# Performance work log

Hardware: AMD Instinct MI355X
Metric: run time of the kernel (lower is better)

Reference implementation:

```python
import jax, jax.numpy as jnp
import numpy as np

C = 32          # mid_channel / in_channel
B = 8           # batch size (number of scenes)
N = 2_000_000   # total points across batch
BN_EPS = 1e-4   # BatchNorm1d eps from norm_fn


def setup_inputs() -> dict:
    key = jax.random.key(0)
    ks = jax.random.split(key, 8)
    s = 0.05
    return {
        "feats": jax.random.normal(ks[0], (N, C), dtype=jnp.float32),
        "batch_idxs": jnp.sort(jax.random.randint(ks[1], (N,), 0, B, dtype=jnp.int32)),
        "off_w1": jax.random.normal(ks[2], (C, C), dtype=jnp.float32) * s,
        "off_b1": jnp.zeros((C,), jnp.float32),
        "bn_gamma": jnp.ones((C,), jnp.float32),   # set_bn_init fills 1.0
        "bn_beta": jnp.zeros((C,), jnp.float32),   # set_bn_init fills 0.0
        "off_w2": jax.random.normal(ks[3], (C, 3), dtype=jnp.float32) * s,
        "off_b2": jnp.zeros((3,), jnp.float32),
        "mask_w1": jax.random.normal(ks[4], (C, C), dtype=jnp.float32) * s,
        "mask_b1": jnp.zeros((C,), jnp.float32),
        "mask_w2": jax.random.normal(ks[5], (C, 1), dtype=jnp.float32) * s,
        "mask_b2": jnp.zeros((1,), jnp.float32),
        "iou_w": jax.random.normal(ks[6], (C, 1), dtype=jnp.float32) * s,
        "iou_b": jnp.zeros((1,), jnp.float32),
    }


def reference(feats, batch_idxs, off_w1, off_b1, bn_gamma, bn_beta, off_w2, off_b2,
              mask_w1, mask_b1, mask_w2, mask_b2, iou_w, iou_b):
    # offset_linear = MLP([C, C, 3], norm_fn=BatchNorm1d): Linear -> BN -> ReLU -> Linear
    h = feats @ off_w1 + off_b1                      # [N, C]
    mu = h.mean(axis=0)
    var = jnp.mean(jnp.square(h - mu), axis=0)       # biased var (torch BN training fwd)
    h = (h - mu) * jax.lax.rsqrt(var + BN_EPS) * bn_gamma + bn_beta
    h = jax.nn.relu(h)
    pt_offsets = h @ off_w2 + off_b2                 # [N, 3]

    # mask_linear = MLP([C, C, 1], norm_fn=None): Linear -> ReLU -> Linear
    m = jax.nn.relu(feats @ mask_w1 + mask_b1)       # [N, C]
    mask_scores = m @ mask_w2 + mask_b2              # [N, 1]

    # global_pool: scatter mean of features over per-batch segments (batch offsets)
    ones = jnp.ones((feats.shape[0],), feats.dtype)
    counts = jax.ops.segment_sum(ones, batch_idxs, num_segments=B)          # [B]
    pooled = jax.ops.segment_sum(feats, batch_idxs, num_segments=B)         # [B, C]
    pooled = pooled / jnp.maximum(counts, 1.0)[:, None]

    # iou_score_linear on the pooled proposal feature
    iou_scores = pooled @ iou_w + iou_b              # [B, 1]
    return pt_offsets, mask_scores, pooled, iou_scores
```

## Files before the change

### kernel.cpp

```cpp
#include <hip/hip_runtime.h>

#define TPB 256

typedef __attribute__((ext_vector_type(8))) short short8;
typedef __attribute__((ext_vector_type(4))) float floatx4;

__device__ __forceinline__ unsigned short bf_rne(float f){
    union { float f; unsigned u; } c; c.f = f;
    unsigned r = c.u + 0x7fffu + ((c.u >> 16) & 1u);
    return (unsigned short)(r >> 16);
}
__device__ __forceinline__ unsigned pack_bf(float lo, float hi){
    union { float f; unsigned u; } a, b; a.f = lo; b.f = hi;
    return __builtin_amdgcn_perm(b.u, a.u, 0x07060302u);
}

__global__ void lb_kernel(const int* __restrict__ bidx, int* __restrict__ ws_lb,
                          int N, int B)
{
    const int t = threadIdx.x;
    if (t <= B){
        int lo = 0, hi = N;
        while (lo < hi){
            const int mid = (lo + hi) >> 1;
            if (bidx[mid] < t) lo = mid + 1; else hi = mid;
        }
        ws_lb[t] = lo;
    }
}

__global__ __launch_bounds__(TPB) void pass1_kernel(
    const float* __restrict__ feats, const int* __restrict__ ws_lb,
    const float* __restrict__ w1, const float* __restrict__ b1,
    const float* __restrict__ mw1, const float* __restrict__ mb1,
    const float* __restrict__ mw2, const float* __restrict__ mb2,
    float* __restrict__ mask_out,
    float* __restrict__ ws_sum, float* __restrict__ ws_sq,
    float* __restrict__ ws_pool, int N, int B)
{
    __shared__ float s_stage[TPB/64][1024];
    __shared__ float s_pool[8][32];
    __shared__ float s_sum[32];
    __shared__ float s_sq[32];
    __shared__ int   s_lb[9];

    const int tid  = threadIdx.x;
    const int lane = tid & 63;
    const int wv   = tid >> 6;
    const int p = lane & 15;
    const int q = lane >> 4;

    if (tid < 32){ s_sum[tid] = 0.f; s_sq[tid] = 0.f; }
    ((float*)s_pool)[tid] = 0.f;
    if (tid <= B) s_lb[tid] = ws_lb[tid];
    __syncthreads();

    short8 aw0, aw1, am0, am1;
    floatx4 ci_h0, ci_h1, ci_m0, ci_m1;
    float mw2v[8];
#pragma unroll
    for (int j = 0; j < 8; ++j){
        const int k = q * 8 + j;
        aw0[j] = (short)bf_rne(w1 [k * 32 + p]);
        aw1[j] = (short)bf_rne(w1 [k * 32 + 16 + p]);
        am0[j] = (short)bf_rne(mw1[k * 32 + p]);
        am1[j] = (short)bf_rne(mw1[k * 32 + 16 + p]);
    }
#pragma unroll
    for (int r = 0; r < 4; ++r){
        const int c0 = q * 4 + r, c1 = 16 + q * 4 + r;
        ci_h0[r] = b1[c0];  ci_h1[r] = b1[c1];
        ci_m0[r] = mb1[c0]; ci_m1[r] = mb1[c1];
        mw2v[r] = mw2[c0];  mw2v[4 + r] = mw2[c1];
    }
    const float mb2s = mb2[0];

    float hsum[8] = {0,0,0,0,0,0,0,0};
    float hsq [8] = {0,0,0,0,0,0,0,0};
    float pacc[4] = {0,0,0,0};

    const int ngroups = (N + 31) >> 5;
    const int nw  = gridDim.x * (TPB / 64);
    const int wid = blockIdx.x * (TPB / 64) + wv;
    const int g0  = (int)((long)wid       * ngroups / nw);
    const int gE  = (int)((long)(wid + 1) * ngroups / nw);

    int curb = 0;
    { const int r = g0 << 5; while (curb < B - 1 && r >= s_lb[curb + 1]) curb++; }
    int lbn = s_lb[curb + 1];

    float* sw = &s_stage[wv][0];
    const int wrow  = lane >> 3;
    const int wg    = (lane & 7) ^ wrow;
    const int cbase = (lane & 7) << 2;
    const int wo0 = ( 0 + wrow) * 32 + (wg << 2);
    const int wo1 = ( 8 + wrow) * 32 + (wg << 2);
    const int wo2 = (16 + wrow) * 32 + (wg << 2);
    const int wo3 = (24 + wrow) * 32 + (wg << 2);
    const int e = p & 7;
    const int ra0 = p * 32        + ((((q << 1)    ) ^ e) << 2);
    const int ra1 = p * 32        + ((((q << 1) + 1) ^ e) << 2);
    const int rb0 = (16 + p) * 32 + ((((q << 1)    ) ^ e) << 2);
    const int rb1 = (16 + p) * 32 + ((((q << 1) + 1) ^ e) << 2);

    floatx4 sv0 = {0,0,0,0}, sv1 = {0,0,0,0}, sv2 = {0,0,0,0}, sv3 = {0,0,0,0};
    if (g0 < gE){
        const float* gp = feats + ((size_t)g0 << 10) + (lane << 2);
        const int r = (g0 << 5) + wrow;
        if (r + 24 < N){
            sv0 = *(const floatx4*)(gp);
            sv1 = *(const floatx4*)(gp + 256);
            sv2 = *(const floatx4*)(gp + 512);
            sv3 = *(const floatx4*)(gp + 768);
        } else {
            if (r      < N) sv0 = *(const floatx4*)(gp);
            if (r +  8 < N) sv1 = *(const floatx4*)(gp + 256);
            if (r + 16 < N) sv2 = *(const floatx4*)(gp + 512);
            if (r + 24 < N) sv3 = *(const floatx4*)(gp + 768);
        }
    }

    for (int g = g0; g < gE; ++g){
        *(floatx4*)(sw + wo0) = sv0;
        *(floatx4*)(sw + wo1) = sv1;
        *(floatx4*)(sw + wo2) = sv2;
        *(floatx4*)(sw + wo3) = sv3;

        floatx4 nv0 = {0,0,0,0}, nv1 = {0,0,0,0}, nv2 = {0,0,0,0}, nv3 = {0,0,0,0};
        if (g + 1 < gE){
            const float* gp = feats + ((size_t)(g + 1) << 10) + (lane << 2);
            const int r = ((g + 1) << 5) + wrow;
            if (r + 24 < N){
                nv0 = *(const floatx4*)(gp);
                nv1 = *(const floatx4*)(gp + 256);
                nv2 = *(const floatx4*)(gp + 512);
                nv3 = *(const floatx4*)(gp + 768);
            } else {
                if (r      < N) nv0 = *(const floatx4*)(gp);
                if (r +  8 < N) nv1 = *(const floatx4*)(gp + 256);
                if (r + 16 < N) nv2 = *(const floatx4*)(gp + 512);
                if (r + 24 < N) nv3 = *(const floatx4*)(gp + 768);
            }
        }

        const int r0 = g << 5;
        if (r0 >= lbn){
#pragma unroll
            for (int j = 0; j < 4; ++j){
                if (pacc[j] != 0.f) atomicAdd(&s_pool[curb][cbase + j], pacc[j]);
                pacc[j] = 0.f;
            }
            do { curb++; } while (curb < B - 1 && r0 >= s_lb[curb + 1]);
            lbn = s_lb[curb + 1];
        }
        const bool slow = (r0 + 31 >= lbn) || (r0 + 31 >= N);

        if (!slow){
            pacc[0] += sv0[0] + sv1[0] + sv2[0] + sv3[0];
            pacc[1] += sv0[1] + sv1[1] + sv2[1] + sv3[1];
            pacc[2] += sv0[2] + sv1[2] + sv2[2] + sv3[2];
            pacc[3] += sv0[3] + sv1[3] + sv2[3] + sv3[3];
        } else {
#define SLOWROW(SV, L) { \
            const int row = r0 + (L * 8) + wrow; \
            if (row < N){ \
                int bl = curb; \
                for (int c = curb + 1; c < B; ++c) bl += (row >= s_lb[c]); \
                atomicAdd(&s_pool[bl][cbase + 0], SV[0]); \
                atomicAdd(&s_pool[bl][cbase + 1], SV[1]); \
                atomicAdd(&s_pool[bl][cbase + 2], SV[2]); \
                atomicAdd(&s_pool[bl][cbase + 3], SV[3]); \
            } }
            SLOWROW(sv0, 0) SLOWROW(sv1, 1) SLOWROW(sv2, 2) SLOWROW(sv3, 3)
#undef SLOWROW
        }

        const floatx4 vA0 = *(const floatx4*)(sw + ra0);
        const floatx4 vA1 = *(const floatx4*)(sw + ra1);
        const floatx4 vB0 = *(const floatx4*)(sw + rb0);
        const floatx4 vB1 = *(const floatx4*)(sw + rb1);

        short8 bfA, bfB;
        {
            unsigned* ba = (unsigned*)&bfA;
            ba[0] = pack_bf(vA0[0], vA0[1]); ba[1] = pack_bf(vA0[2], vA0[3]);
            ba[2] = pack_bf(vA1[0], vA1[1]); ba[3] = pack_bf(vA1[2], vA1[3]);
            unsigned* bb = (unsigned*)&bfB;
            bb[0] = pack_bf(vB0[0], vB0[1]); bb[1] = pack_bf(vB0[2], vB0[3]);
            bb[2] = pack_bf(vB1[0], vB1[1]); bb[3] = pack_bf(vB1[2], vB1[3]);
        }

        const floatx4 chA0 = __builtin_amdgcn_mfma_f32_16x16x32_bf16(aw0, bfA, ci_h0, 0, 0, 0);
        const floatx4 chA1 = __builtin_amdgcn_mfma_f32_16x16x32_bf16(aw1, bfA, ci_h1, 0, 0, 0);
        const floatx4 cmA0 = __builtin_amdgcn_mfma_f32_16x16x32_bf16(am0, bfA, ci_m0, 0, 0, 0);
        const floatx4 cmA1 = __builtin_amdgcn_mfma_f32_16x16x32_bf16(am1, bfA, ci_m1, 0, 0, 0);
        const floatx4 chB0 = __builtin_amdgcn_mfma_f32_16x16x32_bf16(aw0, bfB, ci_h0, 0, 0, 0);
        const floatx4 chB1 = __builtin_amdgcn_mfma_f32_16x16x32_bf16(aw1, bfB, ci_h1, 0, 0, 0);
        const floatx4 cmB0 = __builtin_amdgcn_mfma_f32_16x16x32_bf16(am0, bfB, ci_m0, 0, 0, 0);
        const floatx4 cmB1 = __builtin_amdgcn_mfma_f32_16x16x32_bf16(am1, bfB, ci_m1, 0, 0, 0);

        if (r0 + 31 < N){
#pragma unroll
            for (int r = 0; r < 4; ++r){
                const float a0 = chA0[r], b0 = chB0[r];
                hsum[r] += a0 + b0;
                hsq [r] = fmaf(a0, a0, fmaf(b0, b0, hsq[r]));
                const float a1 = chA1[r], b1v = chB1[r];
                hsum[4 + r] += a1 + b1v;
                hsq [4 + r] = fmaf(a1, a1, fmaf(b1v, b1v, hsq[4 + r]));
            }
        } else {
            if (r0 + p < N){
#pragma unroll
                for (int r = 0; r < 4; ++r){
                    const float a0 = chA0[r]; hsum[r]     += a0; hsq[r]     = fmaf(a0, a0, hsq[r]);
                    const float a1 = chA1[r]; hsum[4 + r] += a1; hsq[4 + r] = fmaf(a1, a1, hsq[4 + r]);
                }
            }
            if (r0 + 16 + p < N){
#pragma unroll
                for (int r = 0; r < 4; ++r){
                    const float b0 = chB0[r]; hsum[r]     += b0; hsq[r]     = fmaf(b0, b0, hsq[r]);
                    const float b1v = chB1[r]; hsum[4 + r] += b1v; hsq[4 + r] = fmaf(b1v, b1v, hsq[4 + r]);
                }
            }
        }

        float tmA = 0.f, tmB = 0.f;
#pragma unroll
        for (int r = 0; r < 4; ++r){
            tmA = fmaf(fmaxf(cmA0[r], 0.f), mw2v[r],     tmA);
            tmA = fmaf(fmaxf(cmA1[r], 0.f), mw2v[4 + r], tmA);
            tmB = fmaf(fmaxf(cmB0[r], 0.f), mw2v[r],     tmB);
            tmB = fmaf(fmaxf(cmB1[r], 0.f), mw2v[4 + r], tmB);
        }
        tmA += __shfl_xor(tmA, 16, 64); tmA += __shfl_xor(tmA, 32, 64);
        tmB += __shfl_xor(tmB, 16, 64); tmB += __shfl_xor(tmB, 32, 64);
        if (q == 0 && (r0 + p) < N)      mask_out[r0 + p]      = tmA + mb2s;
        if (q == 0 && (r0 + 16 + p) < N) mask_out[r0 + 16 + p] = tmB + mb2s;

        sv0 = nv0; sv1 = nv1; sv2 = nv2; sv3 = nv3;
    }

#pragma unroll
    for (int j = 0; j < 4; ++j){
        if (pacc[j] != 0.f) atomicAdd(&s_pool[curb][cbase + j], pacc[j]);
    }
#pragma unroll
    for (int i = 0; i < 8; ++i){
        const int ch = (i >> 2) * 16 + q * 4 + (i & 3);
        atomicAdd(&s_sum[ch], hsum[i]);
        atomicAdd(&s_sq[ch],  hsq[i]);
    }
    __syncthreads();
    if (tid < 32){
        atomicAdd(&ws_sum[tid], s_sum[tid]);
        atomicAdd(&ws_sq[tid],  s_sq[tid]);
    }
    {
        const float pv = ((float*)s_pool)[tid];
        if (pv != 0.f) atomicAdd(&ws_pool[tid], pv);
    }
}

__global__ __launch_bounds__(TPB) void pass2_kernel(
    const float* __restrict__ feats, const int* __restrict__ ws_lb,
    const float* __restrict__ w1, const float* __restrict__ b1,
    const float* __restrict__ gamma, const float* __restrict__ beta,
    const float* __restrict__ w2, const float* __restrict__ b2,
    const float* __restrict__ iw, const float* __restrict__ ib,
    const float* __restrict__ ws_sum, const float* __restrict__ ws_sq,
    const float* __restrict__ ws_pool,
    float* __restrict__ pt_out, float* __restrict__ pooled_out,
    float* __restrict__ iou_out, int N, int B)
{
    __shared__ float s_stage[TPB/64][1024];
    __shared__ float s_sc[32];
    __shared__ float s_bp[32];
    __shared__ float s_pooled[256];
    __shared__ int   s_lb[9];

    const int tid  = threadIdx.x;
    const int lane = tid & 63;
    const int wv   = tid >> 6;
    const int p = lane & 15;
    const int q = lane >> 4;

    if (tid < 32){
        const float invN = 1.f / (float)N;
        const float mu  = ws_sum[tid] * invN;
        const float var = ws_sq[tid] * invN - mu * mu;
        const float s   = gamma[tid] * rsqrtf(var + 1e-4f);
        s_sc[tid] = s;
        s_bp[tid] = (b1[tid] - mu) * s + beta[tid];
    }
    if (tid <= B) s_lb[tid] = ws_lb[tid];
    __syncthreads();

    if (blockIdx.x == 0){
        if (tid < B * 32){
            const int bb = tid >> 5;
            const float cnt = fmaxf((float)(s_lb[bb + 1] - s_lb[bb]), 1.f);
            const float pv = ws_pool[tid] / cnt;
            s_pooled[tid]   = pv;
            pooled_out[tid] = pv;
        }
        __syncthreads();
        if (tid < B){
            float acc = ib[0];
#pragma unroll
            for (int i = 0; i < 32; ++i) acc = fmaf(s_pooled[tid * 32 + i], iw[i], acc);
            iou_out[tid] = acc;
        }
    }

    short8 pw0, pw1;
    floatx4 pc0, pc1;
    float w2v[24];
    const float sc0 = s_sc[p], sc1 = s_sc[16 + p];
#pragma unroll
    for (int j = 0; j < 8; ++j){
        const int k = q * 8 + j;
        pw0[j] = (short)bf_rne(w1[k * 32 + p]      * sc0);
        pw1[j] = (short)bf_rne(w1[k * 32 + 16 + p] * sc1);
    }
#pragma unroll
    for (int r = 0; r < 4; ++r){
        pc0[r] = s_bp[q * 4 + r];
        pc1[r] = s_bp[16 + q * 4 + r];
    }
#pragma unroll
    for (int i = 0; i < 8; ++i){
        const int ch = (i >> 2) * 16 + q * 4 + (i & 3);
        w2v[i]      = w2[ch * 3 + 0];
        w2v[8 + i]  = w2[ch * 3 + 1];
        w2v[16 + i] = w2[ch * 3 + 2];
    }
    const float b2v0 = b2[0], b2v1 = b2[1], b2v2 = b2[2];

    const int ngroups = (N + 31) >> 5;
    const int nw  = gridDim.x * (TPB / 64);
    const int wid = blockIdx.x * (TPB / 64) + wv;
    const int g0  = (int)((long)wid       * ngroups / nw);
    const int gE  = (int)((long)(wid + 1) * ngroups / nw);

    float* sw = &s_stage[wv][0];
    const int wrow = lane >> 3;
    const int wg   = (lane & 7) ^ wrow;
    const int wo0 = ( 0 + wrow) * 32 + (wg << 2);
    const int wo1 = ( 8 + wrow) * 32 + (wg << 2);
    const int wo2 = (16 + wrow) * 32 + (wg << 2);
    const int wo3 = (24 + wrow) * 32 + (wg << 2);
    const int e = p & 7;
    const int ra0 = p * 32        + ((((q << 1)    ) ^ e) << 2);
    const int ra1 = p * 32        + ((((q << 1) + 1) ^ e) << 2);
    const int rb0 = (16 + p) * 32 + ((((q << 1)    ) ^ e) << 2);
    const int rb1 = (16 + p) * 32 + ((((q << 1) + 1) ^ e) << 2);

    floatx4 sv0 = {0,0,0,0}, sv1 = {0,0,0,0}, sv2 = {0,0,0,0}, sv3 = {0,0,0,0};
    if (g0 < gE){
        const float* gp = feats + ((size_t)g0 << 10) + (lane << 2);
        const int r = (g0 << 5) + wrow;
        if (r + 24 < N){
            sv0 = *(const floatx4*)(gp);
            sv1 = *(const floatx4*)(gp + 256);
            sv2 = *(const floatx4*)(gp + 512);
            sv3 = *(const floatx4*)(gp + 768);
        } else {
            if (r      < N) sv0 = *(const floatx4*)(gp);
            if (r +  8 < N) sv1 = *(const floatx4*)(gp + 256);
            if (r + 16 < N) sv2 = *(const floatx4*)(gp + 512);
            if (r + 24 < N) sv3 = *(const floatx4*)(gp + 768);
        }
    }

    for (int g = g0; g < gE; ++g){
        *(floatx4*)(sw + wo0) = sv0;
        *(floatx4*)(sw + wo1) = sv1;
        *(floatx4*)(sw + wo2) = sv2;
        *(floatx4*)(sw + wo3) = sv3;

        floatx4 nv0 = {0,0,0,0}, nv1 = {0,0,0,0}, nv2 = {0,0,0,0}, nv3 = {0,0,0,0};
        if (g + 1 < gE){
            const float* gp = feats + ((size_t)(g + 1) << 10) + (lane << 2);
            const int r = ((g + 1) << 5) + wrow;
            if (r + 24 < N){
                nv0 = *(const floatx4*)(gp);
                nv1 = *(const floatx4*)(gp + 256);
                nv2 = *(const floatx4*)(gp + 512);
                nv3 = *(const floatx4*)(gp + 768);
            } else {
                if (r      < N) nv0 = *(const floatx4*)(gp);
                if (r +  8 < N) nv1 = *(const floatx4*)(gp + 256);
                if (r + 16 < N) nv2 = *(const floatx4*)(gp + 512);
                if (r + 24 < N) nv3 = *(const floatx4*)(gp + 768);
            }
        }

        const floatx4 vA0 = *(const floatx4*)(sw + ra0);
        const floatx4 vA1 = *(const floatx4*)(sw + ra1);
        const floatx4 vB0 = *(const floatx4*)(sw + rb0);
        const floatx4 vB1 = *(const floatx4*)(sw + rb1);

        short8 bfA, bfB;
        {
            unsigned* ba = (unsigned*)&bfA;
            ba[0] = pack_bf(vA0[0], vA0[1]); ba[1] = pack_bf(vA0[2], vA0[3]);
            ba[2] = pack_bf(vA1[0], vA1[1]); ba[3] = pack_bf(vA1[2], vA1[3]);
            unsigned* bb = (unsigned*)&bfB;
            bb[0] = pack_bf(vB0[0], vB0[1]); bb[1] = pack_bf(vB0[2], vB0[3]);
            bb[2] = pack_bf(vB1[0], vB1[1]); bb[3] = pack_bf(vB1[2], vB1[3]);
        }

        const floatx4 cA0 = __builtin_amdgcn_mfma_f32_16x16x32_bf16(pw0, bfA, pc0, 0, 0, 0);
        const floatx4 cA1 = __builtin_amdgcn_mfma_f32_16x16x32_bf16(pw1, bfA, pc1, 0, 0, 0);
        const floatx4 cB0 = __builtin_amdgcn_mfma_f32_16x16x32_bf16(pw0, bfB, pc0, 0, 0, 0);
        const floatx4 cB1 = __builtin_amdgcn_mfma_f32_16x16x32_bf16(pw1, bfB, pc1, 0, 0, 0);

        float sA0 = 0.f, sA1 = 0.f, sA2 = 0.f, sB0 = 0.f, sB1 = 0.f, sB2 = 0.f;
#pragma unroll
        for (int r = 0; r < 4; ++r){
            const float a0 = fmaxf(cA0[r], 0.f);
            const float a1 = fmaxf(cA1[r], 0.f);
            sA0 = fmaf(a0, w2v[r],      sA0); sA0 = fmaf(a1, w2v[4 + r],  sA0);
            sA1 = fmaf(a0, w2v[8 + r],  sA1); sA1 = fmaf(a1, w2v[12 + r], sA1);
            sA2 = fmaf(a0, w2v[16 + r], sA2); sA2 = fmaf(a1, w2v[20 + r], sA2);
            const float b0 = fmaxf(cB0[r], 0.f);
            const float b1v = fmaxf(cB1[r], 0.f);
            sB0 = fmaf(b0, w2v[r],      sB0); sB0 = fmaf(b1v, w2v[4 + r],  sB0);
            sB1 = fmaf(b0, w2v[8 + r],  sB1); sB1 = fmaf(b1v, w2v[12 + r], sB1);
            sB2 = fmaf(b0, w2v[16 + r], sB2); sB2 = fmaf(b1v, w2v[20 + r], sB2);
        }
        sA0 += __shfl_xor(sA0, 16, 64); sA0 += __shfl_xor(sA0, 32, 64);
        sA1 += __shfl_xor(sA1, 16, 64); sA1 += __shfl_xor(sA1, 32, 64);
        sA2 += __shfl_xor(sA2, 16, 64); sA2 += __shfl_xor(sA2, 32, 64);
        sB0 += __shfl_xor(sB0, 16, 64); sB0 += __shfl_xor(sB0, 32, 64);
        sB1 += __shfl_xor(sB1, 16, 64); sB1 += __shfl_xor(sB1, 32, 64);
        sB2 += __shfl_xor(sB2, 16, 64); sB2 += __shfl_xor(sB2, 32, 64);

        const int r0 = g << 5;
        const int rA = r0 + p, rB = r0 + 16 + p;
        if (lane < 48 && rA < N){
            float val = (q == 0) ? (sA0 + b2v0) : ((q == 1) ? (sA1 + b2v1) : (sA2 + b2v2));
            pt_out[(size_t)rA * 3 + q] = val;
        }
        if (lane < 48 && rB < N){
            float val = (q == 0) ? (sB0 + b2v0) : ((q == 1) ? (sB1 + b2v1) : (sB2 + b2v2));
            pt_out[(size_t)rB * 3 + q] = val;
        }

        sv0 = nv0; sv1 = nv1; sv2 = nv2; sv3 = nv3;
    }
}

extern "C" void kernel_launch(void* const* d_in, const int* in_sizes, int n_in,
                              void* d_out, int out_size, void* d_ws, size_t ws_size,
                              hipStream_t stream) {
    const float* feats = (const float*)d_in[0];
    const int*   bidx  = (const int*)d_in[1];
    const float* w1    = (const float*)d_in[2];
    const float* b1    = (const float*)d_in[3];
    const float* gamma = (const float*)d_in[4];
    const float* beta  = (const float*)d_in[5];
    const float* w2    = (const float*)d_in[6];
    const float* b2    = (const float*)d_in[7];
    const float* mw1   = (const float*)d_in[8];
    const float* mb1   = (const float*)d_in[9];
    const float* mw2   = (const float*)d_in[10];
    const float* mb2   = (const float*)d_in[11];
    const float* iw    = (const float*)d_in[12];
    const float* ib    = (const float*)d_in[13];

    const int N = in_sizes[0] / 32;
    const int B = (out_size - 4 * N) / 33;

    float* out    = (float*)d_out;
    float* pt     = out;
    float* mask   = out + (size_t)3 * N;
    float* pooled = out + (size_t)4 * N;
    float* iou    = pooled + (size_t)B * 32;

    float* ws      = (float*)d_ws;
    float* ws_sum  = ws;
    float* ws_sq   = ws + 32;
    float* ws_pool = ws + 64;
    int*   ws_lb   = (int*)(ws + 64 + (size_t)B * 32);

    hipMemsetAsync(ws, 0, (size_t)(64 + B * 32) * sizeof(float), stream);

    int dev = 0;
    hipGetDevice(&dev);
    hipDeviceProp_t prop;
    hipGetDeviceProperties(&prop, dev);
    int per1 = 0, per2 = 0;
    hipOccupancyMaxActiveBlocksPerMultiprocessor(&per1, pass1_kernel, TPB, 0);
    hipOccupancyMaxActiveBlocksPerMultiprocessor(&per2, pass2_kernel, TPB, 0);
    int g1 = per1 * prop.multiProcessorCount; if (g1 < 512) g1 = 512;
    int g2 = per2 * prop.multiProcessorCount; if (g2 < 512) g2 = 512;

    lb_kernel<<<1, 64, 0, stream>>>(bidx, ws_lb, N, B);
    pass1_kernel<<<g1, TPB, 0, stream>>>(feats, ws_lb, w1, b1, mw1, mb1, mw2, mb2,
                                         mask, ws_sum, ws_sq, ws_pool, N, B);
    pass2_kernel<<<g2, TPB, 0, stream>>>(feats, ws_lb, w1, b1, gamma, beta, w2, b2,
                                         iw, ib, ws_sum, ws_sq, ws_pool,
                                         pt, pooled, iou, N, B);
}
```

Measured before the change: 455.3 us.

## Compute BN statistics from input Gram matrix and move mask head to pass2

```diff
diff --git a/kernel.cpp b/kernel.cpp
--- a/kernel.cpp
+++ b/kernel.cpp
@@ -1,10 +1,17 @@
 #include <hip/hip_runtime.h>
 
 #define TPB 256
+#define GRID1 1024
+#define GRID2 1024
+#define MSLICES 8
 
 typedef __attribute__((ext_vector_type(8))) short short8;
 typedef __attribute__((ext_vector_type(4))) float floatx4;
 
+__device__ __forceinline__ unsigned short bf_trunc(float f){
+    union { float f; unsigned u; } c; c.f = f;
+    return (unsigned short)(c.u >> 16);
+}
 __device__ __forceinline__ unsigned short bf_rne(float f){
     union { float f; unsigned u; } c; c.f = f;
     unsigned r = c.u + 0x7fffu + ((c.u >> 16) & 1u);
@@ -13,6 +20,9 @@
 __device__ __forceinline__ unsigned pack_bf(float lo, float hi){
     union { float f; unsigned u; } a, b; a.f = lo; b.f = hi;
     return __builtin_amdgcn_perm(b.u, a.u, 0x07060302u);
+}
+__device__ __forceinline__ float bfbits(unsigned short u){
+    union { unsigned u; float f; } c; c.u = ((unsigned)u) << 16; return c.f;
 }
 
 __global__ void lb_kernel(const int* __restrict__ bidx, int* __restrict__ ws_lb,
@@ -31,17 +41,12 @@
 
 __global__ __launch_bounds__(TPB) void pass1_kernel(
     const float* __restrict__ feats, const int* __restrict__ ws_lb,
-    const float* __restrict__ w1, const float* __restrict__ b1,
-    const float* __restrict__ mw1, const float* __restrict__ mb1,
-    const float* __restrict__ mw2, const float* __restrict__ mb2,
-    float* __restrict__ mask_out,
-    float* __restrict__ ws_sum, float* __restrict__ ws_sq,
-    float* __restrict__ ws_pool, int N, int B)
+    float* __restrict__ ws_pool, float* __restrict__ ws_M,
+    int N, int B)
 {
     __shared__ float s_stage[TPB/64][1024];
     __shared__ float s_pool[8][32];
-    __shared__ float s_sum[32];
-    __shared__ float s_sq[32];
+    __shared__ float s_M[3][256];
     __shared__ int   s_lb[9];
 
     const int tid  = threadIdx.x;
@@ -50,34 +55,13 @@
     const int p = lane & 15;
     const int q = lane >> 4;
 
-    if (tid < 32){ s_sum[tid] = 0.f; s_sq[tid] = 0.f; }
     ((float*)s_pool)[tid] = 0.f;
+    for (int i = tid; i < 768; i += TPB) ((float*)s_M)[i] = 0.f;
     if (tid <= B) s_lb[tid] = ws_lb[tid];
     __syncthreads();
 
-    short8 aw0, aw1, am0, am1;
-    floatx4 ci_h0, ci_h1, ci_m0, ci_m1;
-    float mw2v[8];
-#pragma unroll
-    for (int j = 0; j < 8; ++j){
-        const int k = q * 8 + j;
-        aw0[j] = (short)bf_rne(w1 [k * 32 + p]);
-        aw1[j] = (short)bf_rne(w1 [k * 32 + 16 + p]);
-        am0[j] = (short)bf_rne(mw1[k * 32 + p]);
-        am1[j] = (short)bf_rne(mw1[k * 32 + 16 + p]);
-    }
-#pragma unroll
-    for (int r = 0; r < 4; ++r){
-        const int c0 = q * 4 + r, c1 = 16 + q * 4 + r;
-        ci_h0[r] = b1[c0];  ci_h1[r] = b1[c1];
-        ci_m0[r] = mb1[c0]; ci_m1[r] = mb1[c1];
-        mw2v[r] = mw2[c0];  mw2v[4 + r] = mw2[c1];
-    }
-    const float mb2s = mb2[0];
-
-    float hsum[8] = {0,0,0,0,0,0,0,0};
-    float hsq [8] = {0,0,0,0,0,0,0,0};
     float pacc[4] = {0,0,0,0};
+    floatx4 acc00 = {0,0,0,0}, acc01 = {0,0,0,0}, acc11 = {0,0,0,0};
 
     const int ngroups = (N + 31) >> 5;
     const int nw  = gridDim.x * (TPB / 64);
@@ -97,11 +81,6 @@
     const int wo1 = ( 8 + wrow) * 32 + (wg << 2);
     const int wo2 = (16 + wrow) * 32 + (wg << 2);
     const int wo3 = (24 + wrow) * 32 + (wg << 2);
-    const int e = p & 7;
-    const int ra0 = p * 32        + ((((q << 1)    ) ^ e) << 2);
-    const int ra1 = p * 32        + ((((q << 1) + 1) ^ e) << 2);
-    const int rb0 = (16 + p) * 32 + ((((q << 1)    ) ^ e) << 2);
-    const int rb1 = (16 + p) * 32 + ((((q << 1) + 1) ^ e) << 2);
 
     floatx4 sv0 = {0,0,0,0}, sv1 = {0,0,0,0}, sv2 = {0,0,0,0}, sv3 = {0,0,0,0};
     if (g0 < gE){
@@ -175,69 +154,36 @@
 #undef SLOWROW
         }
 
-        const floatx4 vA0 = *(const floatx4*)(sw + ra0);
-        const floatx4 vA1 = *(const floatx4*)(sw + ra1);
-        const floatx4 vB0 = *(const floatx4*)(sw + rb0);
-        const floatx4 vB1 = *(const floatx4*)(sw + rb1);
-
-        short8 bfA, bfB;
-        {
-            unsigned* ba = (unsigned*)&bfA;
-            ba[0] = pack_bf(vA0[0], vA0[1]); ba[1] = pack_bf(vA0[2], vA0[3]);
-            ba[2] = pack_bf(vA1[0], vA1[1]); ba[3] = pack_bf(vA1[2], vA1[3]);
-            unsigned* bb = (unsigned*)&bfB;
-            bb[0] = pack_bf(vB0[0], vB0[1]); bb[1] = pack_bf(vB0[2], vB0[3]);
-            bb[2] = pack_bf(vB1[0], vB1[1]); bb[3] = pack_bf(vB1[2], vB1[3]);
-        }
-
-        const floatx4 chA0 = __builtin_amdgcn_mfma_f32_16x16x32_bf16(aw0, bfA, ci_h0, 0, 0, 0);
-        const floatx4 chA1 = __builtin_amdgcn_mfma_f32_16x16x32_bf16(aw1, bfA, ci_h1, 0, 0, 0);
-        const floatx4 cmA0 = __builtin_amdgcn_mfma_f32_16x16x32_bf16(am0, bfA, ci_m0, 0, 0, 0);
-        const floatx4 cmA1 = __builtin_amdgcn_mfma_f32_16x16x32_bf16(am1, bfA, ci_m1, 0, 0, 0);
-        const floatx4 chB0 = __builtin_amdgcn_mfma_f32_16x16x32_bf16(aw0, bfB, ci_h0, 0, 0, 0);
-        const floatx4 chB1 = __builtin_amdgcn_mfma_f32_16x16x32_bf16(aw1, bfB, ci_h1, 0, 0, 0);
-        const floatx4 cmB0 = __builtin_amdgcn_mfma_f32_16x16x32_bf16(am0, bfB, ci_m0, 0, 0, 0);
-        const floatx4 cmB1 = __builtin_amdgcn_mfma_f32_16x16x32_bf16(am1, bfB, ci_m1, 0, 0, 0);
-
-        if (r0 + 31 < N){
-#pragma unroll
-            for (int r = 0; r < 4; ++r){
-                const float a0 = chA0[r], b0 = chB0[r];
-                hsum[r] += a0 + b0;
-                hsq [r] = fmaf(a0, a0, fmaf(b0, b0, hsq[r]));
-                const float a1 = chA1[r], b1v = chB1[r];
-                hsum[4 + r] += a1 + b1v;
-                hsq [4 + r] = fmaf(a1, a1, fmaf(b1v, b1v, hsq[4 + r]));
+        short8 hi0, lo0, hi1, lo1;
+#pragma unroll
+        for (int j = 0; j < 8; ++j){
+            const int row = q * 8 + j;
+            const int e2  = row & 7;
+            {
+                const int c = p;
+                const float v = sw[row * 32 + ((((c >> 2) ^ e2) << 2) + (c & 3))];
+                const unsigned short hb = bf_trunc(v);
+                hi0[j] = (short)hb;
+                lo0[j] = (short)bf_trunc(v - bfbits(hb));
             }
-        } else {
-            if (r0 + p < N){
-#pragma unroll
-                for (int r = 0; r < 4; ++r){
-                    const float a0 = chA0[r]; hsum[r]     += a0; hsq[r]     = fmaf(a0, a0, hsq[r]);
-                    const float a1 = chA1[r]; hsum[4 + r] += a1; hsq[4 + r] = fmaf(a1, a1, hsq[4 + r]);
-                }
+            {
+                const int c = 16 + p;
+                const float v = sw[row * 32 + ((((c >> 2) ^ e2) << 2) + (c & 3))];
+                const unsigned short hb = bf_trunc(v);
+                hi1[j] = (short)hb;
+                lo1[j] = (short)bf_trunc(v - bfbits(hb));
             }
-            if (r0 + 16 + p < N){
-#pragma unroll
-                for (int r = 0; r < 4; ++r){
-                    const float b0 = chB0[r]; hsum[r]     += b0; hsq[r]     = fmaf(b0, b0, hsq[r]);
-                    const float b1v = chB1[r]; hsum[4 + r] += b1v; hsq[4 + r] = fmaf(b1v, b1v, hsq[4 + r]);
-                }
-            }
-        }
-
-        float tmA = 0.f, tmB = 0.f;
-#pragma unroll
-        for (int r = 0; r < 4; ++r){
-            tmA = fmaf(fmaxf(cmA0[r], 0.f), mw2v[r],     tmA);
-            tmA = fmaf(fmaxf(cmA1[r], 0.f), mw2v[4 + r], tmA);
-            tmB = fmaf(fmaxf(cmB0[r], 0.f), mw2v[r],     tmB);
-            tmB = fmaf(fmaxf(cmB1[r], 0.f), mw2v[4 + r], tmB);
-        }
-        tmA += __shfl_xor(tmA, 16, 64); tmA += __shfl_xor(tmA, 32, 64);
-        tmB += __shfl_xor(tmB, 16, 64); tmB += __shfl_xor(tmB, 32, 64);
-        if (q == 0 && (r0 + p) < N)      mask_out[r0 + p]      = tmA + mb2s;
-        if (q == 0 && (r0 + 16 + p) < N) mask_out[r0 + 16 + p] = tmB + mb2s;
+        }
+
+        acc00 = __builtin_amdgcn_mfma_f32_16x16x32_bf16(hi0, hi0, acc00, 0, 0, 0);
+        acc00 = __builtin_amdgcn_mfma_f32_16x16x32_bf16(hi0, lo0, acc00, 0, 0, 0);
+        acc00 = __builtin_amdgcn_mfma_f32_16x16x32_bf16(lo0, hi0, acc00, 0, 0, 0);
+        acc01 = __builtin_amdgcn_mfma_f32_16x16x32_bf16(hi0, hi1, acc01, 0, 0, 0);
+        acc01 = __builtin_amdgcn_mfma_f32_16x16x32_bf16(hi0, lo1, acc01, 0, 0, 0);
+        acc01 = __builtin_amdgcn_mfma_f32_16x16x32_bf16(lo0, hi1, acc01, 0, 0, 0);
+        acc11 = __builtin_amdgcn_mfma_f32_16x16x32_bf16(hi1, hi1, acc11, 0, 0, 0);
+        acc11 = __builtin_amdgcn_mfma_f32_16x16x32_bf16(hi1, lo1, acc11, 0, 0, 0);
+        acc11 = __builtin_amdgcn_mfma_f32_16x16x32_bf16(lo1, hi1, acc11, 0, 0, 0);
 
         sv0 = nv0; sv1 = nv1; sv2 = nv2; sv3 = nv3;
     }
@@ -247,34 +193,44 @@
         if (pacc[j] != 0.f) atomicAdd(&s_pool[curb][cbase + j], pacc[j]);
     }
 #pragma unroll
-    for (int i = 0; i < 8; ++i){
-        const int ch = (i >> 2) * 16 + q * 4 + (i & 3);
-        atomicAdd(&s_sum[ch], hsum[i]);
-        atomicAdd(&s_sq[ch],  hsq[i]);
+    for (int r = 0; r < 4; ++r){
+        const int idx = (4 * q + r) * 16 + p;
+        atomicAdd(&s_M[0][idx], acc00[r]);
+        atomicAdd(&s_M[1][idx], acc01[r]);
+        atomicAdd(&s_M[2][idx], acc11[r]);
     }
     __syncthreads();
-    if (tid < 32){
-        atomicAdd(&ws_sum[tid], s_sum[tid]);
-        atomicAdd(&ws_sq[tid],  s_sq[tid]);
-    }
     {
         const float pv = ((float*)s_pool)[tid];
         if (pv != 0.f) atomicAdd(&ws_pool[tid], pv);
     }
+    {
+        float* slice = ws_M + (size_t)(blockIdx.x % MSLICES) * 768;
+        for (int i = tid; i < 768; i += TPB){
+            const float v = ((float*)s_M)[i];
+            if (v != 0.f) atomicAdd(slice + i, v);
+        }
+    }
 }
 
 __global__ __launch_bounds__(TPB) void pass2_kernel(
     const float* __restrict__ feats, const int* __restrict__ ws_lb,
-    const float* __restrict__ w1, const float* __restrict__ b1,
+    const float* __restrict__ w1,
     const float* __restrict__ gamma, const float* __restrict__ beta,
     const float* __restrict__ w2, const float* __restrict__ b2,
+    const float* __restrict__ mw1, const float* __restrict__ mb1,
+    const float* __restrict__ mw2, const float* __restrict__ mb2,
     const float* __restrict__ iw, const float* __restrict__ ib,
-    const float* __restrict__ ws_sum, const float* __restrict__ ws_sq,
-    const float* __restrict__ ws_pool,
-    float* __restrict__ pt_out, float* __restrict__ pooled_out,
-    float* __restrict__ iou_out, int N, int B)
+    const float* __restrict__ ws_pool, const float* __restrict__ ws_M,
+    float* __restrict__ pt_out, float* __restrict__ mask_out,
+    float* __restrict__ pooled_out, float* __restrict__ iou_out,
+    int N, int B)
 {
     __shared__ float s_stage[TPB/64][1024];
+    __shared__ float s_w[1024];
+    __shared__ float s_M2[1024];
+    __shared__ float s_mu[32];
+    __shared__ float s_var[32];
     __shared__ float s_sc[32];
     __shared__ float s_bp[32];
     __shared__ float s_pooled[256];
@@ -286,15 +242,52 @@
     const int p = lane & 15;
     const int q = lane >> 4;
 
+    for (int i = tid; i < 1024; i += TPB) s_w[i] = w1[i];
+    for (int i = tid; i < 256; i += TPB){
+        float v0 = 0.f, v1 = 0.f, v2 = 0.f;
+#pragma unroll
+        for (int s = 0; s < MSLICES; ++s){
+            v0 += ws_M[(size_t)s * 768 + i];
+            v1 += ws_M[(size_t)s * 768 + 256 + i];
+            v2 += ws_M[(size_t)s * 768 + 512 + i];
+        }
+        const int m = i >> 4, n = i & 15;
+        s_M2[m * 32 + n] = v0;
+        s_M2[(16 + m) * 32 + 16 + n] = v2;
+        s_M2[m * 32 + 16 + n] = v1;
+        s_M2[(16 + n) * 32 + m] = v1;
+    }
     if (tid < 32){
-        const float invN = 1.f / (float)N;
-        const float mu  = ws_sum[tid] * invN;
-        const float var = ws_sq[tid] * invN - mu * mu;
+        float s = 0.f;
+        for (int b = 0; b < B; ++b) s += ws_pool[b * 32 + tid];
+        s_mu[tid]  = s / (float)N;
+        s_var[tid] = 0.f;
+    }
+    if (tid <= B) s_lb[tid] = ws_lb[tid];
+    __syncthreads();
+
+    {
+        const int c = tid & 31, a0 = (tid >> 5) * 4;
+        float part = 0.f;
+#pragma unroll
+        for (int a = a0; a < a0 + 4; ++a){
+            float t2 = 0.f;
+#pragma unroll
+            for (int b = 0; b < 32; ++b) t2 = fmaf(s_w[b * 32 + c], s_M2[a * 32 + b], t2);
+            part = fmaf(s_w[a * 32 + c], t2, part);
+        }
+        atomicAdd(&s_var[c], part);
+    }
+    __syncthreads();
+    if (tid < 32){
+        float muh = 0.f;
+#pragma unroll
+        for (int a = 0; a < 32; ++a) muh = fmaf(s_mu[a], s_w[a * 32 + tid], muh);
+        const float var = s_var[tid] / (float)N - muh * muh;
         const float s   = gamma[tid] * rsqrtf(var + 1e-4f);
         s_sc[tid] = s;
-        s_bp[tid] = (b1[tid] - mu) * s + beta[tid];
-    }
-    if (tid <= B) s_lb[tid] = ws_lb[tid];
+        s_bp[tid] = beta[tid] - muh * s;
+    }
     __syncthreads();
 
     if (blockIdx.x == 0){
@@ -314,20 +307,24 @@
         }
     }
 
-    short8 pw0, pw1;
-    floatx4 pc0, pc1;
-    float w2v[24];
+    short8 aw0, aw1, am0, am1;
+    floatx4 ci_h0, ci_h1, ci_m0, ci_m1;
+    float mw2v[8], w2v[24];
     const float sc0 = s_sc[p], sc1 = s_sc[16 + p];
 #pragma unroll
     for (int j = 0; j < 8; ++j){
         const int k = q * 8 + j;
-        pw0[j] = (short)bf_rne(w1[k * 32 + p]      * sc0);
-        pw1[j] = (short)bf_rne(w1[k * 32 + 16 + p] * sc1);
+        aw0[j] = (short)bf_rne(s_w[k * 32 + p]      * sc0);
+        aw1[j] = (short)bf_rne(s_w[k * 32 + 16 + p] * sc1);
+        am0[j] = (short)bf_rne(mw1[k * 32 + p]);
+        am1[j] = (short)bf_rne(mw1[k * 32 + 16 + p]);
     }
 #pragma unroll
     for (int r = 0; r < 4; ++r){
-        pc0[r] = s_bp[q * 4 + r];
-        pc1[r] = s_bp[16 + q * 4 + r];
+        const int c0 = q * 4 + r, c1 = 16 + q * 4 + r;
+        ci_h0[r] = s_bp[c0];  ci_h1[r] = s_bp[c1];
+        ci_m0[r] = mb1[c0];   ci_m1[r] = mb1[c1];
+        mw2v[r] = mw2[c0];    mw2v[4 + r] = mw2[c1];
     }
 #pragma unroll
     for (int i = 0; i < 8; ++i){
@@ -337,6 +334,7 @@
         w2v[16 + i] = w2[ch * 3 + 2];
     }
     const float b2v0 = b2[0], b2v1 = b2[1], b2v2 = b2[2];
+    const float mb2s = mb2[0];
 
     const int ngroups = (N + 31) >> 5;
     const int nw  = gridDim.x * (TPB / 64);
@@ -412,12 +410,17 @@
             bb[2] = pack_bf(vB1[0], vB1[1]); bb[3] = pack_bf(vB1[2], vB1[3]);
         }
 
-        const floatx4 cA0 = __builtin_amdgcn_mfma_f32_16x16x32_bf16(pw0, bfA, pc0, 0, 0, 0);
-        const floatx4 cA1 = __builtin_amdgcn_mfma_f32_16x16x32_bf16(pw1, bfA, pc1, 0, 0, 0);
-        const floatx4 cB0 = __builtin_amdgcn_mfma_f32_16x16x32_bf16(pw0, bfB, pc0, 0, 0, 0);
-        const floatx4 cB1 = __builtin_amdgcn_mfma_f32_16x16x32_bf16(pw1, bfB, pc1, 0, 0, 0);
+        const floatx4 cA0 = __builtin_amdgcn_mfma_f32_16x16x32_bf16(aw0, bfA, ci_h0, 0, 0, 0);
+        const floatx4 cA1 = __builtin_amdgcn_mfma_f32_16x16x32_bf16(aw1, bfA, ci_h1, 0, 0, 0);
+        const floatx4 mA0 = __builtin_amdgcn_mfma_f32_16x16x32_bf16(am0, bfA, ci_m0, 0, 0, 0);
+        const floatx4 mA1 = __builtin_amdgcn_mfma_f32_16x16x32_bf16(am1, bfA, ci_m1, 0, 0, 0);
+        const floatx4 cB0 = __builtin_amdgcn_mfma_f32_16x16x32_bf16(aw0, bfB, ci_h0, 0, 0, 0);
+        const floatx4 cB1 = __builtin_amdgcn_mfma_f32_16x16x32_bf16(aw1, bfB, ci_h1, 0, 0, 0);
+        const floatx4 mB0 = __builtin_amdgcn_mfma_f32_16x16x32_bf16(am0, bfB, ci_m0, 0, 0, 0);
+        const floatx4 mB1 = __builtin_amdgcn_mfma_f32_16x16x32_bf16(am1, bfB, ci_m1, 0, 0, 0);
 
         float sA0 = 0.f, sA1 = 0.f, sA2 = 0.f, sB0 = 0.f, sB1 = 0.f, sB2 = 0.f;
+        float tmA = 0.f, tmB = 0.f;
 #pragma unroll
         for (int r = 0; r < 4; ++r){
             const float a0 = fmaxf(cA0[r], 0.f);
@@ -430,6 +433,10 @@
             sB0 = fmaf(b0, w2v[r],      sB0); sB0 = fmaf(b1v, w2v[4 + r],  sB0);
             sB1 = fmaf(b0, w2v[8 + r],  sB1); sB1 = fmaf(b1v, w2v[12 + r], sB1);
             sB2 = fmaf(b0, w2v[16 + r], sB2); sB2 = fmaf(b1v, w2v[20 + r], sB2);
+            tmA = fmaf(fmaxf(mA0[r], 0.f), mw2v[r],     tmA);
+            tmA = fmaf(fmaxf(mA1[r], 0.f), mw2v[4 + r], tmA);
+            tmB = fmaf(fmaxf(mB0[r], 0.f), mw2v[r],     tmB);
+            tmB = fmaf(fmaxf(mB1[r], 0.f), mw2v[4 + r], tmB);
         }
         sA0 += __shfl_xor(sA0, 16, 64); sA0 += __shfl_xor(sA0, 32, 64);
         sA1 += __shfl_xor(sA1, 16, 64); sA1 += __shfl_xor(sA1, 32, 64);
@@ -437,17 +444,21 @@
         sB0 += __shfl_xor(sB0, 16, 64); sB0 += __shfl_xor(sB0, 32, 64);
         sB1 += __shfl_xor(sB1, 16, 64); sB1 += __shfl_xor(sB1, 32, 64);
         sB2 += __shfl_xor(sB2, 16, 64); sB2 += __shfl_xor(sB2, 32, 64);
+        tmA += __shfl_xor(tmA, 16, 64); tmA += __shfl_xor(tmA, 32, 64);
+        tmB += __shfl_xor(tmB, 16, 64); tmB += __shfl_xor(tmB, 32, 64);
 
         const int r0 = g << 5;
         const int rA = r0 + p, rB = r0 + 16 + p;
         if (lane < 48 && rA < N){
-            float val = (q == 0) ? (sA0 + b2v0) : ((q == 1) ? (sA1 + b2v1) : (sA2 + b2v2));
+            const float val = (q == 0) ? (sA0 + b2v0) : ((q == 1) ? (sA1 + b2v1) : (sA2 + b2v2));
             pt_out[(size_t)rA * 3 + q] = val;
         }
         if (lane < 48 && rB < N){
-            float val = (q == 0) ? (sB0 + b2v0) : ((q == 1) ? (sB1 + b2v1) : (sB2 + b2v2));
+            const float val = (q == 0) ? (sB0 + b2v0) : ((q == 1) ? (sB1 + b2v1) : (sB2 + b2v2));
             pt_out[(size_t)rB * 3 + q] = val;
         }
+        if (q == 0 && rA < N) mask_out[rA] = tmA + mb2s;
+        if (q == 0 && rB < N) mask_out[rB] = tmB + mb2s;
 
         sv0 = nv0; sv1 = nv1; sv2 = nv2; sv3 = nv3;
     }
@@ -470,6 +481,7 @@
     const float* mb2   = (const float*)d_in[11];
     const float* iw    = (const float*)d_in[12];
     const float* ib    = (const float*)d_in[13];
+    (void)b1;
 
     const int N = in_sizes[0] / 32;
     const int B = (out_size - 4 * N) / 33;
@@ -481,27 +493,16 @@
     float* iou    = pooled + (size_t)B * 32;
 
     float* ws      = (float*)d_ws;
-    float* ws_sum  = ws;
-    float* ws_sq   = ws + 32;
-    float* ws_pool = ws + 64;
-    int*   ws_lb   = (int*)(ws + 64 + (size_t)B * 32);
-
-    hipMemsetAsync(ws, 0, (size_t)(64 + B * 32) * sizeof(float), stream);
-
-    int dev = 0;
-    hipGetDevice(&dev);
-    hipDeviceProp_t prop;
-    hipGetDeviceProperties(&prop, dev);
-    int per1 = 0, per2 = 0;
-    hipOccupancyMaxActiveBlocksPerMultiprocessor(&per1, pass1_kernel, TPB, 0);
-    hipOccupancyMaxActiveBlocksPerMultiprocessor(&per2, pass2_kernel, TPB, 0);
-    int g1 = per1 * prop.multiProcessorCount; if (g1 < 512) g1 = 512;
-    int g2 = per2 * prop.multiProcessorCount; if (g2 < 512) g2 = 512;
+    float* ws_pool = ws;
+    float* ws_M    = ws + 256;
+    int*   ws_lb   = (int*)(ws + 256 + MSLICES * 768);
+
+    (void)hipMemsetAsync(ws, 0, (size_t)(256 + MSLICES * 768) * sizeof(float), stream);
 
     lb_kernel<<<1, 64, 0, stream>>>(bidx, ws_lb, N, B);
-    pass1_kernel<<<g1, TPB, 0, stream>>>(feats, ws_lb, w1, b1, mw1, mb1, mw2, mb2,
-                                         mask, ws_sum, ws_sq, ws_pool, N, B);
-    pass2_kernel<<<g2, TPB, 0, stream>>>(feats, ws_lb, w1, b1, gamma, beta, w2, b2,
-                                         iw, ib, ws_sum, ws_sq, ws_pool,
-                                         pt, pooled, iou, N, B);
-}
+    pass1_kernel<<<GRID1, TPB, 0, stream>>>(feats, ws_lb, ws_pool, ws_M, N, B);
+    pass2_kernel<<<GRID2, TPB, 0, stream>>>(feats, ws_lb, w1, gamma, beta, w2, b2,
+                                            mw1, mb1, mw2, mb2, iw, ib,
+                                            ws_pool, ws_M,
+                                            pt, mask, pooled, iou, N, B);
+}
```

New measurement: 470.0 us. +3.2%, slower.
